# Kernel tuning notes

Hardware: AMD Instinct MI355X
Metric: run time of the kernel (lower is better)

## Reference

```python
import jax, jax.numpy as jnp
import numpy as np
from jax import lax

B, L, C = 128, 16384, 12      # batch, signal length, ECG channels
D = 128                        # latent_size
K, STRIDE = 64, 64             # encoder conv
TI, TO, TIG = 64, 8, 0         # timesteps_in / out / ignore


def setup_inputs() -> dict:
    key = jax.random.key(0)
    ks = jax.random.split(key, 7)
    s = 0.05
    X = jax.random.normal(ks[0], (B, L, C), jnp.float32)
    conv_w = jax.random.normal(ks[1], (D, C, K), jnp.float32) * s
    conv_b = jnp.zeros((D,), jnp.float32)
    W_ih = jax.random.normal(ks[2], (3 * D, D), jnp.float32) * s
    W_hh = jax.random.normal(ks[3], (3 * D, D), jnp.float32) * s
    b_ih = jnp.zeros((3 * D,), jnp.float32)
    b_hh = jnp.zeros((3 * D,), jnp.float32)
    pred_W = jax.random.normal(ks[4], (TO, D, D), jnp.float32) * s
    pred_b = jnp.zeros((TO, D), jnp.float32)
    return {"X": X, "conv_w": conv_w, "conv_b": conv_b, "W_ih": W_ih,
            "W_hh": W_hh, "b_ih": b_ih, "b_hh": b_hh,
            "pred_W": pred_W, "pred_b": pred_b}


def _gru(enc, W_ih, W_hh, b_ih, b_hh):
    # enc: [T, B, D] -> context [T, B, D], final hidden [B, D]
    def step(h, xt):
        gi = xt @ W_ih.T + b_ih              # [B, 3D]
        gh = h @ W_hh.T + b_hh
        ir, iz, inn = jnp.split(gi, 3, axis=-1)
        hr, hz, hn = jnp.split(gh, 3, axis=-1)
        r = jax.nn.sigmoid(ir + hr)
        z = jax.nn.sigmoid(iz + hz)
        n = jnp.tanh(inn + r * hn)
        h_new = (1.0 - z) * n + z * h
        return h_new, h_new
    h0 = jnp.zeros((enc.shape[1], enc.shape[2]), enc.dtype)
    hT, ctx = lax.scan(step, h0, enc)
    return ctx, hT


def reference(X, conv_w, conv_b, W_ih, W_hh, b_ih, b_hh, pred_W, pred_b):
    # X: [B, L, C] -> [B, C, L]
    x = X.transpose(0, 2, 1)
    z = lax.conv_general_dilated(x, conv_w, (STRIDE,), 'VALID',
                                 dimension_numbers=('NCH', 'OIH', 'NCH'))
    z = jax.nn.relu(z + conv_b[None, :, None])     # [B, D, T]
    enc = z.transpose(2, 0, 1)                     # [T, B, D]
    ctx, hT = _gru(enc, W_ih, W_hh, b_ih, b_hh)    # [T, B, D]

    T = enc.shape[0]
    S = T - TI - (TO + TIG + 1)                    # prediction steps per offset
    ctx_s = ctx[TI:TI + S]                         # [S, B, D]
    # predictor per offset i: ctx_s @ W[i].T + b[i]  -> [O, S, B, D]
    pred = jnp.einsum('sbd,oed->osbe', ctx_s, pred_W) + pred_b[:, None, None, :]
    # encoded targets enc[TI+i+1 : TI+i+1+S] for each offset i -> [O, S, B, D]
    idx = TI + 1 + jnp.arange(TO)[:, None] + jnp.arange(S)[None, :]
    tgt = enc[idx]
    # scores[o,s,b,c] = <encoded_latent[b], pred_latent[c]>
    scores = jnp.einsum('osbd,oscd->osbc', tgt, pred)
    logsm = jax.nn.log_softmax(scores, axis=-1)
    diag = jnp.diagonal(logsm, axis1=-2, axis2=-1)  # [O, S, B]
    denom = jnp.float32(B * TO * S)
    loss = -jnp.sum(diag) / denom
    correct = jnp.sum(jnp.argmax(logsm, axis=-2) == jnp.arange(B)[None, None, :])
    accuracy = correct.astype(jnp.float32) / denom
    hidden = hT[None]                               # [1, B, D]
    return accuracy, loss, hidden
```

## Files before the change

### kernel.cpp

```cpp
#include <hip/hip_runtime.h>
#include <math.h>

typedef __attribute__((ext_vector_type(8))) short bf16x8;
typedef __attribute__((ext_vector_type(4))) float f32x4;

#define Bdim 128
#define Cdim 12
#define Ddim 128
#define Tdim 256
#define TOn  8
#define TIn  64
#define Sn   183
#define DENOMF 187392.0f
#define NEG_INF -3.402823466e38f

#define OFFB_ENC 0
#define OFFB_CTX 8388608
#define OFFB_GI  16777216
#define OFFB_BCT 67108864
#define OFFB_WT  67305472
#define OFFB_LP  67403776
#define OFFB_CP  67409632
#define OFFB_WHP 67415488

__device__ __forceinline__ float frcp(float x) { return __builtin_amdgcn_rcpf(x); }

__device__ __forceinline__ unsigned short f2b(float x) {
    unsigned int u = __builtin_bit_cast(unsigned int, x);
    u += 0x7FFFu + ((u >> 16) & 1u);
    return (unsigned short)(u >> 16);
}
__device__ __forceinline__ unsigned int pk2(float a, float b) {
    return (unsigned int)f2b(a) | ((unsigned int)f2b(b) << 16);
}
__device__ __forceinline__ float b2f_lo(unsigned int w) {
    return __builtin_bit_cast(float, w << 16);
}
__device__ __forceinline__ float b2f_hi(unsigned int w) {
    return __builtin_bit_cast(float, w & 0xffff0000u);
}

__device__ __forceinline__ uint4 ldg4u_pin(const unsigned int* p) {
    uint4 r;
    asm volatile("global_load_dwordx4 %0, %1, off\n\ts_waitcnt vmcnt(0)"
                 : "=v"(r) : "v"(p) : "memory");
    return r;
}

__device__ __forceinline__ void dot2b(float& acc, unsigned int a, unsigned int b) {
    asm("v_dot2_f32_bf16 %0, %1, %2, %0" : "+v"(acc) : "v"(a), "v"(b));
}

__global__ __launch_bounds__(256) void k_prep(const float* __restrict__ conv_w,
                                              unsigned short* __restrict__ BcT,
                                              const float* __restrict__ W_ih,
                                              unsigned short* __restrict__ Wt,
                                              const float* __restrict__ W_hh,
                                              unsigned int* __restrict__ Whp) {
    int id = blockIdx.x * 256 + threadIdx.x;
    if (id < 128 * 768) {
        int d = id / 768, klin = id % 768;
        int kt = klin / 12, c = klin % 12;
        BcT[id] = f2b(conv_w[d * 768 + c * 64 + kt]);
    }
    if (id < 384 * 128) Wt[id] = f2b(W_ih[id]);
    if (id < 384 * 64) {
        int row = id >> 6, k2 = id & 63;
        Whp[id] = pk2(W_hh[row * 128 + 2 * k2], W_hh[row * 128 + 2 * k2 + 1]);
    }
}

__global__ __launch_bounds__(256) void k_conv(const float* __restrict__ X,
                                              const unsigned short* __restrict__ BcT,
                                              const float* __restrict__ conv_b,
                                              unsigned short* __restrict__ encb) {
    const int t = blockIdx.x;
    __shared__ __align__(16) char As[16384];
    __shared__ __align__(16) char Bs[16384];
    const int tid = threadIdx.x;
    const int lane = tid & 63, wid = tid >> 6;
    const int wy = wid >> 1, wx = wid & 1;
    const int g = lane >> 4, ln = lane & 15;

    f32x4 acc[4][4];
#pragma unroll
    for (int i = 0; i < 4; ++i)
#pragma unroll
        for (int j = 0; j < 4; ++j) acc[i][j] = (f32x4){0.f, 0.f, 0.f, 0.f};

    for (int kc = 0; kc < 768; kc += 64) {
        __syncthreads();
#pragma unroll
        for (int it = 0; it < 4; ++it) {
            int G = tid + it * 256;
            int r = G >> 3, go = G & 7;
            const float* src = X + (size_t)r * (16384 * 12) + t * 768 + kc + go * 8;
            float4 f0 = *(const float4*)src;
            float4 f1 = *(const float4*)(src + 4);
            uint4 w; w.x = pk2(f0.x, f0.y); w.y = pk2(f0.z, f0.w);
            w.z = pk2(f1.x, f1.y); w.w = pk2(f1.z, f1.w);
            *(uint4*)(As + (r * 8 + (go ^ (r & 7))) * 16) = w;
            uint4 v = *(const uint4*)(BcT + (size_t)r * 768 + kc + go * 8);
            *(uint4*)(Bs + (r * 8 + (go ^ (r & 7))) * 16) = v;
        }
        __syncthreads();
#pragma unroll
        for (int ks = 0; ks < 2; ++ks) {
            bf16x8 af[4], bfr[4];
            const int kb = ks * 64 + g * 16;
#pragma unroll
            for (int mi = 0; mi < 4; ++mi) {
                int r = wy * 64 + mi * 16 + ln;
                af[mi] = *(const bf16x8*)(As + r * 128 + (kb ^ ((r & 7) << 4)));
            }
#pragma unroll
            for (int ni = 0; ni < 4; ++ni) {
                int r = wx * 64 + ni * 16 + ln;
                bfr[ni] = *(const bf16x8*)(Bs + r * 128 + (kb ^ ((r & 7) << 4)));
            }
#pragma unroll
            for (int mi = 0; mi < 4; ++mi)
#pragma unroll
                for (int ni = 0; ni < 4; ++ni)
                    acc[mi][ni] = __builtin_amdgcn_mfma_f32_16x16x32_bf16(af[mi], bfr[ni], acc[mi][ni], 0, 0, 0);
        }
    }
    float cb[4];
#pragma unroll
    for (int ni = 0; ni < 4; ++ni) cb[ni] = conv_b[wx * 64 + ni * 16 + ln];
    unsigned short* dst = encb + (size_t)t * (128 * 128);
#pragma unroll
    for (int mi = 0; mi < 4; ++mi)
#pragma unroll
        for (int jj = 0; jj < 4; ++jj) {
            int b = wy * 64 + mi * 16 + g * 4 + jj;
#pragma unroll
            for (int ni = 0; ni < 4; ++ni) {
                int d = wx * 64 + ni * 16 + ln;
                dst[b * 128 + d] = f2b(fmaxf(acc[mi][ni][jj] + cb[ni], 0.f));
            }
        }
}

__global__ __launch_bounds__(256) void k_gi(const unsigned short* __restrict__ encb,
                                            const unsigned short* __restrict__ Wt,
                                            const float* __restrict__ b_ih,
                                            float* __restrict__ gi) {
    const int mt = blockIdx.x, nt = blockIdx.y;
    __shared__ __align__(16) char As[32768];
    __shared__ __align__(16) char Bs[32768];
    const int tid = threadIdx.x;
    const int lane = tid & 63, wid = tid >> 6;
    const int wy = wid >> 1, wx = wid & 1;
    const int g = lane >> 4, ln = lane & 15;

    {
        const unsigned short* asrc = encb + (size_t)mt * (128 * 128);
        const unsigned short* bsrc = Wt + (size_t)nt * (128 * 128);
#pragma unroll
        for (int it = 0; it < 8; ++it) {
            int G = tid + it * 256;
            int r = G >> 4, go = G & 15;
            *(uint4*)(As + (r * 16 + (go ^ (r & 7))) * 16) = *(const uint4*)(asrc + r * 128 + go * 8);
            *(uint4*)(Bs + (r * 16 + (go ^ (r & 7))) * 16) = *(const uint4*)(bsrc + r * 128 + go * 8);
        }
    }
    __syncthreads();

    f32x4 acc[4][4];
#pragma unroll
    for (int i = 0; i < 4; ++i)
#pragma unroll
        for (int j = 0; j < 4; ++j) acc[i][j] = (f32x4){0.f, 0.f, 0.f, 0.f};
#pragma unroll
    for (int ks = 0; ks < 4; ++ks) {
        bf16x8 af[4], bfr[4];
        const int kb = ks * 64 + g * 16;
#pragma unroll
        for (int mi = 0; mi < 4; ++mi) {
            int r = wy * 64 + mi * 16 + ln;
            af[mi] = *(const bf16x8*)(As + r * 256 + (kb ^ ((r & 7) << 4)));
        }
#pragma unroll
        for (int ni = 0; ni < 4; ++ni) {
            int r = wx * 64 + ni * 16 + ln;
            bfr[ni] = *(const bf16x8*)(Bs + r * 256 + (kb ^ ((r & 7) << 4)));
        }
#pragma unroll
        for (int mi = 0; mi < 4; ++mi)
#pragma unroll
            for (int ni = 0; ni < 4; ++ni)
                acc[mi][ni] = __builtin_amdgcn_mfma_f32_16x16x32_bf16(af[mi], bfr[ni], acc[mi][ni], 0, 0, 0);
    }
    float bv[4];
#pragma unroll
    for (int ni = 0; ni < 4; ++ni) bv[ni] = b_ih[nt * 128 + wx * 64 + ni * 16 + ln];
#pragma unroll
    for (int mi = 0; mi < 4; ++mi)
#pragma unroll
        for (int jj = 0; jj < 4; ++jj) {
            int m = mt * 128 + wy * 64 + mi * 16 + g * 4 + jj;
#pragma unroll
            for (int ni = 0; ni < 4; ++ni) {
                int n = nt * 128 + wx * 64 + ni * 16 + ln;
                gi[(size_t)m * 384 + n] = acc[mi][ni][jj] + bv[ni];
            }
        }
}

__global__ __launch_bounds__(512, 2) void k_gru(const float* __restrict__ gi,
                                                const unsigned int* __restrict__ Whp,
                                                const float* __restrict__ bhh,
                                                unsigned int* __restrict__ ctxp,
                                                float* __restrict__ out_hidden) {
    const int b = blockIdx.x;
    const int tid = threadIdx.x;
    const int g = tid >> 2, q = tid & 3;
    __shared__ unsigned int hbuf[2][4][72];

    uint4 w0[4], w1[4], w2[4];
    {
        const unsigned int* W0 = Whp + (size_t)g * 64 + q * 16;
        const unsigned int* W1 = Whp + (size_t)(g + 128) * 64 + q * 16;
        const unsigned int* W2 = Whp + (size_t)(g + 256) * 64 + q * 16;
#pragma unroll
        for (int i = 0; i < 4; ++i) {
            w0[i] = ldg4u_pin(W0 + i * 4);
            w1[i] = ldg4u_pin(W1 + i * 4);
            w2[i] = ldg4u_pin(W2 + i * 4);
        }
    }
    const float bh0 = bhh[g], bh1 = bhh[g + 128], bh2 = bhh[g + 256];

    hbuf[0][q][g >> 1] = 0u;

    float p0r = gi[(size_t)b * 384 + g];
    float p0z = gi[(size_t)b * 384 + 128 + g];
    float p0n = gi[(size_t)b * 384 + 256 + g];
    float p1r = gi[((size_t)128 + b) * 384 + g];
    float p1z = gi[((size_t)128 + b) * 384 + 128 + g];
    float p1n = gi[((size_t)128 + b) * 384 + 256 + g];
    __syncthreads();

    for (int t = 0; t < 256; ++t) {
        const int cur = t & 1;
        float p2r = 0.f, p2z = 0.f, p2n = 0.f;
        if (t + 2 < 256) {
            const float* gp = gi + ((size_t)(t + 2) * 128 + b) * 384;
            p2r = gp[g]; p2z = gp[128 + g]; p2n = gp[256 + g];
        }

        const unsigned int* hc = &hbuf[cur][q][q * 16];
        uint4 h2[4];
#pragma unroll
        for (int i = 0; i < 4; ++i) h2[i] = *(const uint4*)(hc + i * 4);
        unsigned int hw = hbuf[cur][q][g >> 1];
        const float hold = (g & 1) ? b2f_hi(hw) : b2f_lo(hw);

        float a0 = 0.f, a1 = 0.f, a2 = 0.f;
#pragma unroll
        for (int i = 0; i < 4; ++i) {
            dot2b(a0, w0[i].x, h2[i].x); dot2b(a1, w1[i].x, h2[i].x); dot2b(a2, w2[i].x, h2[i].x);
            dot2b(a0, w0[i].y, h2[i].y); dot2b(a1, w1[i].y, h2[i].y); dot2b(a2, w2[i].y, h2[i].y);
            dot2b(a0, w0[i].z, h2[i].z); dot2b(a1, w1[i].z, h2[i].z); dot2b(a2, w2[i].z, h2[i].z);
            dot2b(a0, w0[i].w, h2[i].w); dot2b(a1, w1[i].w, h2[i].w); dot2b(a2, w2[i].w, h2[i].w);
        }
        a0 += __shfl_xor(a0, 1); a0 += __shfl_xor(a0, 2);
        a1 += __shfl_xor(a1, 1); a1 += __shfl_xor(a1, 2);
        a2 += __shfl_xor(a2, 1); a2 += __shfl_xor(a2, 2);

        float xr = p0r + a0 + bh0;  xr = fminf(fmaxf(xr, -60.f), 60.f);
        float xz = p0z + a1 + bh1;  xz = fminf(fmaxf(xz, -60.f), 60.f);
        float r = frcp(1.f + __expf(-xr));
        float z = frcp(1.f + __expf(-xz));
        float xn = p0n + r * (a2 + bh2); xn = fminf(fmaxf(xn, -15.f), 15.f);
        float e2 = __expf(-2.f * xn);
        float n = (1.f - e2) * frcp(1.f + e2);
        float hnew = (1.f - z) * n + z * hold;

        float hn2 = __shfl_down(hnew, 4);
        if (!(g & 1)) {
            unsigned int pw = pk2(hnew, hn2);
            hbuf[cur ^ 1][q][g >> 1] = pw;
            if (q == 0) {
                ctxp[((size_t)t * 128 + b) * 64 + (g >> 1)] = pw;
                if (t == 255) {
                    out_hidden[b * 128 + g] = hnew;
                    out_hidden[b * 128 + g + 1] = hn2;
                }
            }
        }
        p0r = p1r; p0z = p1z; p0n = p1n;
        p1r = p2r; p1z = p2z; p1n = p2n;
        __syncthreads();
    }
}

__global__ __launch_bounds__(256) void k_cpc(const unsigned short* __restrict__ ctxb,
                                             const unsigned short* __restrict__ encb,
                                             const float* __restrict__ pW,
                                             const float* __restrict__ pb,
                                             float* __restrict__ lp,
                                             float* __restrict__ cp) {
    const int s = blockIdx.x, o = blockIdx.y;
    __shared__ __align__(16) char bufA[32768];
    __shared__ __align__(16) char bufB[32768];
    __shared__ float rowm[2][128], rowsum[2][128];
    __shared__ float Lrow[128], diagv[128];
    __shared__ float colv[2][128];
    __shared__ int   colix[2][128];
    __shared__ float fin[4];

    const int tid = threadIdx.x;
    const int lane = tid & 63, wid = tid >> 6;
    const int wy = wid >> 1, wx = wid & 1;
    const int g = lane >> 4, ln = lane & 15;

    {
        const unsigned short* src = ctxb + (size_t)(TIn + s) * (128 * 128);
        const float* wsrc = pW + (size_t)o * (128 * 128);
#pragma unroll
        for (int it = 0; it < 8; ++it) {
            int G = tid + it * 256;
            int r = G >> 4, go = G & 15;
            *(uint4*)(bufA + (r * 16 + (go ^ (r & 7))) * 16) = *(const uint4*)(src + r * 128 + go * 8);
            float4 f0 = *(const float4*)(wsrc + r * 128 + go * 8);
            float4 f1 = *(const float4*)(wsrc + r * 128 + go * 8 + 4);
            uint4 w; w.x = pk2(f0.x, f0.y); w.y = pk2(f0.z, f0.w);
            w.z = pk2(f1.x, f1.y); w.w = pk2(f1.z, f1.w);
            *(uint4*)(bufB + (r * 16 + (go ^ (r & 7))) * 16) = w;
        }
    }
    __syncthreads();

    f32x4 acc[4][4];
#pragma unroll
    for (int i = 0; i < 4; ++i)
#pragma unroll
        for (int j = 0; j < 4; ++j) acc[i][j] = (f32x4){0.f, 0.f, 0.f, 0.f};
#pragma unroll
    for (int ks = 0; ks < 4; ++ks) {
        bf16x8 af[4], bfr[4];
        const int kb = ks * 64 + g * 16;
#pragma unroll
        for (int mi = 0; mi < 4; ++mi) {
            int r = wy * 64 + mi * 16 + ln;
            af[mi] = *(const bf16x8*)(bufB + r * 256 + (kb ^ ((r & 7) << 4)));
        }
#pragma unroll
        for (int ni = 0; ni < 4; ++ni) {
            int r = wx * 64 + ni * 16 + ln;
            bfr[ni] = *(const bf16x8*)(bufA + r * 256 + (kb ^ ((r & 7) << 4)));
        }
#pragma unroll
        for (int mi = 0; mi < 4; ++mi)
#pragma unroll
            for (int ni = 0; ni < 4; ++ni)
                acc[mi][ni] = __builtin_amdgcn_mfma_f32_16x16x32_bf16(af[mi], bfr[ni], acc[mi][ni], 0, 0, 0);
    }
    __syncthreads();

    {
        float pbv[4][4];
#pragma unroll
        for (int mi = 0; mi < 4; ++mi) {
            int e0 = wy * 64 + mi * 16 + g * 4;
#pragma unroll
            for (int jj = 0; jj < 4; ++jj) pbv[mi][jj] = pb[o * 128 + e0 + jj];
        }
#pragma unroll
        for (int mi = 0; mi < 4; ++mi) {
            int e0 = wy * 64 + mi * 16 + g * 4;
#pragma unroll
            for (int ni = 0; ni < 4; ++ni) {
                int c = wx * 64 + ni * 16 + ln;
                unsigned int lo = pk2(acc[mi][ni][0] + pbv[mi][0], acc[mi][ni][1] + pbv[mi][1]);
                unsigned int hi = pk2(acc[mi][ni][2] + pbv[mi][2], acc[mi][ni][3] + pbv[mi][3]);
                int byteoff = c * 256 + ((e0 * 2) ^ ((c & 7) << 4));
                *(uint2*)(bufB + byteoff) = make_uint2(lo, hi);
            }
        }
        const unsigned short* tsrc = encb + (size_t)(TIn + 1 + o + s) * (128 * 128);
#pragma unroll
        for (int it = 0; it < 8; ++it) {
            int G = tid + it * 256;
            int r = G >> 4, go = G & 15;
            *(uint4*)(bufA + (r * 16 + (go ^ (r & 7))) * 16) = *(const uint4*)(tsrc + r * 128 + go * 8);
        }
    }
    __syncthreads();

#pragma unroll
    for (int i = 0; i < 4; ++i)
#pragma unroll
        for (int j = 0; j < 4; ++j) acc[i][j] = (f32x4){0.f, 0.f, 0.f, 0.f};
#pragma unroll
    for (int ks = 0; ks < 4; ++ks) {
        bf16x8 af[4], bfr[4];
        const int kb = ks * 64 + g * 16;
#pragma unroll
        for (int mi = 0; mi < 4; ++mi) {
            int r = wy * 64 + mi * 16 + ln;
            af[mi] = *(const bf16x8*)(bufA + r * 256 + (kb ^ ((r & 7) << 4)));
        }
#pragma unroll
        for (int ni = 0; ni < 4; ++ni) {
            int r = wx * 64 + ni * 16 + ln;
            bfr[ni] = *(const bf16x8*)(bufB + r * 256 + (kb ^ ((r & 7) << 4)));
        }
#pragma unroll
        for (int mi = 0; mi < 4; ++mi)
#pragma unroll
            for (int ni = 0; ni < 4; ++ni)
                acc[mi][ni] = __builtin_amdgcn_mfma_f32_16x16x32_bf16(af[mi], bfr[ni], acc[mi][ni], 0, 0, 0);
    }

#pragma unroll
    for (int mi = 0; mi < 4; ++mi) {
#pragma unroll
        for (int jj = 0; jj < 4; ++jj) {
            float m = fmaxf(fmaxf(acc[mi][0][jj], acc[mi][1][jj]),
                            fmaxf(acc[mi][2][jj], acc[mi][3][jj]));
            m = fmaxf(m, __shfl_xor(m, 1)); m = fmaxf(m, __shfl_xor(m, 2));
            m = fmaxf(m, __shfl_xor(m, 4)); m = fmaxf(m, __shfl_xor(m, 8));
            float sm = __expf(acc[mi][0][jj] - m) + __expf(acc[mi][1][jj] - m)
                     + __expf(acc[mi][2][jj] - m) + __expf(acc[mi][3][jj] - m);
            sm += __shfl_xor(sm, 1); sm += __shfl_xor(sm, 2);
            sm += __shfl_xor(sm, 4); sm += __shfl_xor(sm, 8);
            int b = wy * 64 + mi * 16 + g * 4 + jj;
            if (ln == 0) { rowm[wx][b] = m; rowsum[wx][b] = sm; }
            if (wy == wx && ln == g * 4 + jj) diagv[b] = acc[mi][mi][jj];
        }
    }
    __syncthreads();
    if (tid < 128) {
        float m0 = rowm[0][tid], m1 = rowm[1][tid];
        float mm = fmaxf(m0, m1);
        float ss = rowsum[0][tid] * __expf(m0 - mm) + rowsum[1][tid] * __expf(m1 - mm);
        Lrow[tid] = mm + __logf(ss);
    }
    __syncthreads();

    float Lr[4][4];
#pragma unroll
    for (int mi = 0; mi < 4; ++mi)
#pragma unroll
        for (int jj = 0; jj < 4; ++jj) Lr[mi][jj] = Lrow[wy * 64 + mi * 16 + g * 4 + jj];

#pragma unroll
    for (int ni = 0; ni < 4; ++ni) {
        float best = NEG_INF; int bidx = 0x7fffffff;
#pragma unroll
        for (int mi = 0; mi < 4; ++mi)
#pragma unroll
            for (int jj = 0; jj < 4; ++jj) {
                float v = acc[mi][ni][jj] - Lr[mi][jj];
                int r = wy * 64 + mi * 16 + g * 4 + jj;
                if (v > best) { best = v; bidx = r; }
            }
#pragma unroll
        for (int mask = 16; mask <= 32; mask <<= 1) {
            float ov = __shfl_xor(best, mask);
            int   oi = __shfl_xor(bidx, mask);
            if (ov > best || (ov == best && oi < bidx)) { best = ov; bidx = oi; }
        }
        if (g == 0) {
            int c = wx * 64 + ni * 16 + ln;
            colv[wy][c] = best; colix[wy][c] = bidx;
        }
    }
    __syncthreads();

    float lsum = 0.f, csum = 0.f;
    if (tid < 128) {
        lsum = diagv[tid] - Lrow[tid];
        float v0 = colv[0][tid], v1 = colv[1][tid];
        int ix = (v1 > v0) ? colix[1][tid] : colix[0][tid];
        csum = (ix == tid) ? 1.f : 0.f;
    }
#pragma unroll
    for (int off = 32; off > 0; off >>= 1) {
        lsum += __shfl_down(lsum, off);
        csum += __shfl_down(csum, off);
    }
    if (lane == 0 && wid < 2) { fin[wid] = lsum; fin[2 + wid] = csum; }
    __syncthreads();
    if (tid == 0) {
        lp[o * Sn + s] = fin[0] + fin[1];
        cp[o * Sn + s] = fin[2] + fin[3];
    }
}

__global__ __launch_bounds__(256) void k_final(const float* __restrict__ lp,
                                               const float* __restrict__ cp,
                                               float* __restrict__ out) {
    __shared__ float sl[256], sc2[256];
    const int tid = threadIdx.x;
    float l = 0.f, c = 0.f;
    for (int i = tid; i < TOn * Sn; i += 256) { l += lp[i]; c += cp[i]; }
    sl[tid] = l; sc2[tid] = c;
    __syncthreads();
    for (int s = 128; s > 0; s >>= 1) {
        if (tid < s) { sl[tid] += sl[tid + s]; sc2[tid] += sc2[tid + s]; }
        __syncthreads();
    }
    if (tid == 0) {
        out[0] = sc2[0] / DENOMF;
        out[1] = -sl[0] / DENOMF;
    }
}

extern "C" void kernel_launch(void* const* d_in, const int* in_sizes, int n_in,
                              void* d_out, int out_size, void* d_ws, size_t ws_size,
                              hipStream_t stream) {
    const float* X      = (const float*)d_in[0];
    const float* conv_w = (const float*)d_in[1];
    const float* conv_b = (const float*)d_in[2];
    const float* W_ih   = (const float*)d_in[3];
    const float* W_hh   = (const float*)d_in[4];
    const float* b_ih   = (const float*)d_in[5];
    const float* b_hh   = (const float*)d_in[6];
    const float* pred_W = (const float*)d_in[7];
    const float* pred_b = (const float*)d_in[8];
    float* out = (float*)d_out;
    char*  ws  = (char*)d_ws;

    unsigned short* encb = (unsigned short*)(ws + OFFB_ENC);
    unsigned short* ctxb = (unsigned short*)(ws + OFFB_CTX);
    float*          gi   = (float*)(ws + OFFB_GI);
    unsigned short* BcT  = (unsigned short*)(ws + OFFB_BCT);
    unsigned short* Wt   = (unsigned short*)(ws + OFFB_WT);
    float*          lp   = (float*)(ws + OFFB_LP);
    float*          cp   = (float*)(ws + OFFB_CP);
    unsigned int*   Whp  = (unsigned int*)(ws + OFFB_WHP);

    k_prep <<<dim3(384),     dim3(256), 0, stream>>>(conv_w, BcT, W_ih, Wt, W_hh, Whp);
    k_conv <<<dim3(256),     dim3(256), 0, stream>>>(X, BcT, conv_b, encb);
    k_gi   <<<dim3(256, 3),  dim3(256), 0, stream>>>(encb, Wt, b_ih, gi);
    k_gru  <<<dim3(128),     dim3(512), 0, stream>>>(gi, Whp, b_hh, (unsigned int*)ctxb, out + 2);
    k_cpc  <<<dim3(Sn, TOn), dim3(256), 0, stream>>>(ctxb, encb, pred_W, pred_b, lp, cp);
    k_final<<<dim3(1),       dim3(256), 0, stream>>>(lp, cp, out);
}
```

Before: 271.8 us.

## Stream GRU input gates into LDS ring buffer via async global-to-LDS loads

The GRU recurrence stops prefetching per-step input-gate values into registers from global memory. Instead, 96 threads issue async global_load_lds copies into a 4-slot LDS ring three steps ahead, and all threads read their r/z/n inputs from LDS. The per-step barrier becomes manual vmcnt/lgkmcnt waits plus s_barrier, intended to take global load latency off the serial recurrence path. The gain depends on the hand-written wait counts being correct, which adds a risk of races or stale data, and it costs extra LDS plus a dummy slot for out-of-range steps.

```diff
diff --git a/kernel.cpp b/kernel.cpp
--- a/kernel.cpp
+++ b/kernel.cpp
@@ -43,6 +43,12 @@
 __device__ __forceinline__ uint4 ldg4u_pin(const unsigned int* p) {
     uint4 r;
     asm volatile("global_load_dwordx4 %0, %1, off\n\ts_waitcnt vmcnt(0)"
+                 : "=v"(r) : "v"(p) : "memory");
+    return r;
+}
+__device__ __forceinline__ float ldgf_pin(const float* p) {
+    float r;
+    asm volatile("global_load_dword %0, %1, off\n\ts_waitcnt vmcnt(0)"
                  : "=v"(r) : "v"(p) : "memory");
     return r;
 }
@@ -208,15 +214,17 @@
         }
 }
 
-__global__ __launch_bounds__(512, 2) void k_gru(const float* __restrict__ gi,
-                                                const unsigned int* __restrict__ Whp,
-                                                const float* __restrict__ bhh,
-                                                unsigned int* __restrict__ ctxp,
-                                                float* __restrict__ out_hidden) {
+__global__ __launch_bounds__(512, 2)
+void k_gru(const float* __restrict__ gi,
+           const unsigned int* __restrict__ Whp,
+           const float* __restrict__ bhh,
+           unsigned int* __restrict__ ctxp,
+           float* __restrict__ out_hidden) {
     const int b = blockIdx.x;
     const int tid = threadIdx.x;
     const int g = tid >> 2, q = tid & 3;
     __shared__ unsigned int hbuf[2][4][72];
+    __shared__ __align__(16) float giL[5][384];
 
     uint4 w0[4], w1[4], w2[4];
     {
@@ -230,25 +238,42 @@
             w2[i] = ldg4u_pin(W2 + i * 4);
         }
     }
-    const float bh0 = bhh[g], bh1 = bhh[g + 128], bh2 = bhh[g + 256];
-
-    hbuf[0][q][g >> 1] = 0u;
-
-    float p0r = gi[(size_t)b * 384 + g];
-    float p0z = gi[(size_t)b * 384 + 128 + g];
-    float p0n = gi[(size_t)b * 384 + 256 + g];
-    float p1r = gi[((size_t)128 + b) * 384 + g];
-    float p1z = gi[((size_t)128 + b) * 384 + 128 + g];
-    float p1n = gi[((size_t)128 + b) * 384 + 256 + g];
-    __syncthreads();
+    const float bh0 = ldgf_pin(bhh + g);
+    const float bh1 = ldgf_pin(bhh + 128 + g);
+    const float bh2 = ldgf_pin(bhh + 256 + g);
+
+    if (!(g & 1)) hbuf[0][q][g >> 1] = 0u;
+
+    if (tid < 96) {
+#pragma unroll
+        for (int s = 0; s < 3; ++s) {
+            const float* src = gi + ((size_t)s * 128 + b) * 384 + tid * 4;
+            __builtin_amdgcn_global_load_lds(
+                (const __attribute__((address_space(1))) unsigned int*)src,
+                (__attribute__((address_space(3))) unsigned int*)&giL[s][(tid >> 6) << 8],
+                16, 0, 0);
+        }
+    }
+    if (tid < 128) asm volatile("s_waitcnt vmcnt(2)" ::: "memory");
+    asm volatile("s_waitcnt lgkmcnt(0)" ::: "memory");
+    __builtin_amdgcn_s_barrier();
 
     for (int t = 0; t < 256; ++t) {
         const int cur = t & 1;
-        float p2r = 0.f, p2z = 0.f, p2n = 0.f;
-        if (t + 2 < 256) {
-            const float* gp = gi + ((size_t)(t + 2) * 128 + b) * 384;
-            p2r = gp[g]; p2z = gp[128 + g]; p2n = gp[256 + g];
-        }
+        if (tid < 96) {
+            const int nt = t + 3;
+            const int slot = (nt < 256) ? (nt & 3) : 4;
+            const int srct = (nt < 256) ? nt : 0;
+            const float* src = gi + ((size_t)srct * 128 + b) * 384 + tid * 4;
+            __builtin_amdgcn_global_load_lds(
+                (const __attribute__((address_space(1))) unsigned int*)src,
+                (__attribute__((address_space(3))) unsigned int*)&giL[slot][(tid >> 6) << 8],
+                16, 0, 0);
+        }
+        const float* gslot = giL[t & 3];
+        const float p0r = gslot[g];
+        const float p0z = gslot[128 + g];
+        const float p0n = gslot[256 + g];
 
         const unsigned int* hc = &hbuf[cur][q][q * 16];
         uint4 h2[4];
@@ -290,9 +315,9 @@
                 }
             }
         }
-        p0r = p1r; p0z = p1z; p0n = p1n;
-        p1r = p2r; p1z = p2z; p1n = p2n;
-        __syncthreads();
+        if (tid < 128) asm volatile("s_waitcnt vmcnt(2)" ::: "memory");
+        asm volatile("s_waitcnt lgkmcnt(0)" ::: "memory");
+        __builtin_amdgcn_s_barrier();
     }
 }
 
```

After: 285.3 us. +5.0%, slower.
